# Performance work log

Measured on AMD Instinct MI355X. Metric: run time of the kernel, lower is better.

## Reference

```python
import jax, jax.numpy as jnp
import numpy as np

H = 512          # hidden_size
SH = 120         # scoring_net_hidden_size
B = 1024         # batch
S = 64           # num_sentences


def setup_inputs() -> dict:
    key = jax.random.key(0)
    ks = jax.random.split(key, 12)
    sc = 0.05
    return {
        "C": jax.random.normal(ks[0], (B, S, H), jnp.float32),
        "Q": jax.random.normal(ks[1], (B, 1, H), jnp.float32),
        "prev_M": jax.random.normal(ks[2], (B, 1, H), jnp.float32),
        # scoring network params: fc1: 4H -> SH, fc2: SH -> 1
        "fc1_w": jax.random.normal(ks[3], (SH, 4 * H), jnp.float32) * sc,
        "fc1_b": jnp.zeros((SH,), jnp.float32),
        "fc2_w": jax.random.normal(ks[4], (1, SH), jnp.float32) * sc,
        "fc2_b": jnp.zeros((1,), jnp.float32),
        # GRU params (torch layout: rows ordered r, z, n)
        "W_ih": jax.random.normal(ks[5], (3 * H, H), jnp.float32) * sc,
        "W_hh": jax.random.normal(ks[6], (3 * H, H), jnp.float32) * sc,
        "b_ih": jnp.zeros((3 * H,), jnp.float32),
        "b_hh": jnp.zeros((3 * H,), jnp.float32),
    }


def reference(C, Q, prev_M, fc1_w, fc1_b, fc2_w, fc2_b, W_ih, W_hh, b_ih, b_hh):
    # --- scoring network (arch=1 feature vector) ---
    feat = jnp.concatenate(
        [C * Q, C * prev_M, jnp.abs(C - Q), jnp.abs(C - prev_M)], axis=2
    )  # [B, S, 4H]
    h1 = jnp.tanh(jnp.einsum("bsf,kf->bsk", feat, fc1_w) + fc1_b)
    G = jax.nn.sigmoid((jnp.einsum("bsk,ok->bso", h1, fc2_w) + fc2_b)[..., 0])  # [B, S]

    # --- gated GRU memory update over sentences ---
    xg_all = jnp.einsum("bsh,gh->bsg", C, W_ih) + b_ih  # [B, S, 3H] precomputed input gates

    def step(h, inp):
        xg, g = inp  # xg: [B, 3H], g: [B]
        hg = h @ W_hh.T + b_hh
        xr, xz, xn = jnp.split(xg, 3, axis=-1)
        hr, hz, hn = jnp.split(hg, 3, axis=-1)
        r = jax.nn.sigmoid(xr + hr)
        z = jax.nn.sigmoid(xz + hz)
        n = jnp.tanh(xn + r * hn)
        h_gru = (1.0 - z) * n + z * h          # standard torch GRU update
        g = g[:, None]
        h_new = g * h_gru + (1.0 - g) * h      # episodic gating
        return h_new, None

    h0 = jnp.zeros((C.shape[0], H), C.dtype)
    h_final, _ = jax.lax.scan(step, h0, (xg_all.transpose(1, 0, 2), G.T))
    return h_final[:, None, :]  # [B, 1, H]
```

## Files before the change

kernel.cpp:

```cpp
#include <hip/hip_runtime.h>
#include <hip/hip_bf16.h>

#define H_ 512
#define SH_ 120
#define B_ 1024
#define S_ 64

typedef __bf16 bf16x8 __attribute__((ext_vector_type(8)));
typedef float floatx4 __attribute__((ext_vector_type(4)));

__device__ __forceinline__ float bf2f(ushort u) {
    union { unsigned int i; float f; } v; v.i = ((unsigned int)u) << 16; return v.f;
}
__device__ __forceinline__ ushort f2bf(float f) {
    union { float f; unsigned int i; } v; v.f = f;
    unsigned int x = v.i;
    unsigned int r = (x + 0x7fffu + ((x >> 16) & 1u)) >> 16;
    return (ushort)r;
}

__device__ __attribute__((aligned(64))) unsigned g_prog[256];

__global__ __launch_bounds__(256) void prep_w(
    const float* __restrict__ fc1w, ushort* __restrict__ fc1wb,
    const float* __restrict__ Wih,  ushort* __restrict__ Wihb,
    const float* __restrict__ Whh,  ushort* __restrict__ Whhb)
{
    const int stride = gridDim.x * blockDim.x;
    const int tid = blockIdx.x * blockDim.x + threadIdx.x;
    for (int i = tid; i < 61440; i += stride) {
        const float4 v = ((const float4*)fc1w)[i];
        ushort4 o; o.x = f2bf(v.x); o.y = f2bf(v.y); o.z = f2bf(v.z); o.w = f2bf(v.w);
        ((ushort4*)fc1wb)[i] = o;
    }
    for (int i = tid; i < 196608; i += stride) {
        const float4 v = ((const float4*)Wih)[i];
        ushort4 o; o.x = f2bf(v.x); o.y = f2bf(v.y); o.z = f2bf(v.z); o.w = f2bf(v.w);
        ((ushort4*)Wihb)[i] = o;
    }
    for (int i = tid; i < 196608; i += stride) {
        const float4 v = ((const float4*)Whh)[i];
        ushort4 o; o.x = f2bf(v.x); o.y = f2bf(v.y); o.z = f2bf(v.z); o.w = f2bf(v.w);
        ((ushort4*)Whhb)[i] = o;
    }
}

__global__ __launch_bounds__(256) void g_kernel(
    const float* __restrict__ C, const float* __restrict__ Q,
    const float* __restrict__ M, const ushort* __restrict__ fc1wb,
    const float* __restrict__ fc1b, const float* __restrict__ fc2w,
    const float* __restrict__ fc2b, float* __restrict__ G)
{
    __shared__ float qrow[H_];
    __shared__ float mrow[H_];
    __shared__ __align__(16) ushort featT[64 * 72];
    __shared__ __align__(16) ushort wT[128 * 72];
    __shared__ float h1s[64 * 132];

    const int b = blockIdx.x;
    const int t = threadIdx.x;
    for (int i = t; i < H_; i += 256) { qrow[i] = Q[(size_t)b * H_ + i]; mrow[i] = M[(size_t)b * H_ + i]; }

    const int wrow = t >> 1;
    const int wc0  = (t & 1) * 32;
    if (wrow >= SH_) {
        uint4* dst = (uint4*)&wT[wrow * 72 + wc0];
        const uint4 z = {0u, 0u, 0u, 0u};
        dst[0] = z; dst[1] = z; dst[2] = z; dst[3] = z;
    }
    __syncthreads();

    const int lane = t & 63;
    const int wv   = t >> 6;
    const int quad = lane >> 4;
    const int l15  = lane & 15;
    const int arow = wv * 16 + l15;
    const int s    = t >> 2;
    const int c0   = (t & 3) * 16;

    floatx4 acc[8];
#pragma unroll
    for (int i = 0; i < 8; ++i) acc[i] = (floatx4){0.f, 0.f, 0.f, 0.f};

    for (int hc = 0; hc < H_; hc += 64) {
        float cr[16];
        {
            const float4* csrc = (const float4*)(C + ((size_t)b * S_ + s) * H_ + hc + c0);
            *(float4*)&cr[0]  = csrc[0];
            *(float4*)&cr[4]  = csrc[1];
            *(float4*)&cr[8]  = csrc[2];
            *(float4*)&cr[12] = csrc[3];
        }
#pragma unroll
        for (int seg = 0; seg < 4; ++seg) {
#pragma unroll
            for (int u = 0; u < 16; ++u) {
                const int kk = c0 + u;
                const float c = cr[u];
                const float o = (seg == 0 || seg == 2) ? qrow[hc + kk] : mrow[hc + kk];
                const float v = (seg < 2) ? c * o : fabsf(c - o);
                featT[s * 72 + kk] = f2bf(v);
            }
            if (wrow < SH_) {
                const uint4* src = (const uint4*)(fc1wb + (size_t)wrow * (4 * H_) + seg * H_ + hc + wc0);
                uint4* dst = (uint4*)&wT[wrow * 72 + wc0];
                dst[0] = src[0]; dst[1] = src[1]; dst[2] = src[2]; dst[3] = src[3];
            }
            __syncthreads();
#pragma unroll
            for (int ks = 0; ks < 64; ks += 32) {
                const int ao = ks + quad * 8;
                const bf16x8 af = *(const bf16x8*)&featT[arow * 72 + ao];
#pragma unroll
                for (int nt = 0; nt < 8; ++nt) {
                    const bf16x8 bfr = *(const bf16x8*)&wT[(nt * 16 + l15) * 72 + ao];
                    acc[nt] = __builtin_amdgcn_mfma_f32_16x16x32_bf16(af, bfr, acc[nt], 0, 0, 0);
                }
            }
            __syncthreads();
        }
    }

#pragma unroll
    for (int nt = 0; nt < 8; ++nt) {
        const int col = nt * 16 + l15;
        const float bias = (col < SH_) ? fc1b[col] : 0.f;
#pragma unroll
        for (int r = 0; r < 4; ++r) {
            const int row = wv * 16 + quad * 4 + r;
            h1s[row * 132 + col] = (col < SH_) ? tanhf(acc[nt][r] + bias) : 0.f;
        }
    }
    __syncthreads();
    {
        const int part = t & 3;
        float sum = 0.f;
        for (int k = part; k < SH_; k += 4) sum += h1s[s * 132 + k] * fc2w[k];
        sum += __shfl_xor(sum, 1);
        sum += __shfl_xor(sum, 2);
        if (part == 0) {
            const float logit = sum + fc2b[0];
            G[(size_t)b * S_ + s] = 1.f / (1.f + expf(-logit));
        }
    }
}

__global__ __launch_bounds__(256) void scan_all(
    const float* __restrict__ C, const ushort* __restrict__ Wihb,
    const ushort* __restrict__ Whhb, const float* __restrict__ bih,
    const float* __restrict__ bhh, const float* __restrict__ G,
    uint* __restrict__ hp0, uint* __restrict__ hp1,
    float* __restrict__ out)
{
    __shared__ __align__(16) ushort Whh_s[96 * 520];
    __shared__ __align__(16) ushort As[3 * 64 * 72];
    __shared__ __align__(16) ushort Wih_s[96 * 72];

    const int bx = blockIdx.x;
    const int jt = bx >> 4;
    const int bt = ((bx & 7) << 1) | ((bx >> 3) & 1);
    const int jb = jt * 32;
    const int bb = bt * 64;
    const int t  = threadIdx.x;
    const int lane = t & 63;
    const int wv   = t >> 6;
    const int quad = lane >> 4;
    const int l15  = lane & 15;
    const int arow = wv * 16 + l15;
    const int crow = t >> 2;
    const int cc0  = (t & 3) * 16;
    const int hrow = t >> 2;
    const int hseg = t & 3;

    const unsigned vbase = __hip_atomic_load(&g_prog[(bt << 4) + jt],
                                             __ATOMIC_RELAXED, __HIP_MEMORY_SCOPE_AGENT);

#pragma unroll
    for (int i = 0; i < 24; ++i) {
        const int gid = i * 256 + t;
        const int row = gid >> 6;
        const int grp = gid & 63;
        const int grow = (row >> 5) * H_ + jb + (row & 31);
        *(uint4*)&Whh_s[row * 520 + grp * 8] =
            *(const uint4*)(Whhb + (size_t)grow * H_ + grp * 8);
    }

    float br_[2], bz_[2], bxn_[2], bhn_[2];
#pragma unroll
    for (int nt = 0; nt < 2; ++nt) {
        const int j = jb + nt * 16 + l15;
        br_[nt]  = bih[j] + bhh[j];
        bz_[nt]  = bih[H_ + j] + bhh[H_ + j];
        bxn_[nt] = bih[2 * H_ + j];
        bhn_[nt] = bhh[2 * H_ + j];
    }

    const int hold_kc  = (jb >> 6) << 6;
    const int hold_off = jb & 63;

    const uint* hr = hp0;
    uint*       hw = hp1;

    float cr[16];
    unsigned long long hreg[8];
    uint4 wreg[3];

    auto load_cw = [&](int tstep, int kc) {
        const float4* src = (const float4*)(C + ((size_t)(bb + crow) * S_ + tstep) * H_ + kc + cc0);
        *(float4*)&cr[0]  = src[0];
        *(float4*)&cr[4]  = src[1];
        *(float4*)&cr[8]  = src[2];
        *(float4*)&cr[12] = src[3];
#pragma unroll
        for (int i = 0; i < 3; ++i) {
            const int gid = i * 256 + t;
            const int row = gid >> 3;
            const int grp = gid & 7;
            const int grow = (row >> 5) * H_ + jb + (row & 31);
            wreg[i] = *(const uint4*)(Wihb + (size_t)grow * H_ + kc + grp * 8);
        }
    };
    auto load_h = [&](int kc) {
        const unsigned long long* src = (const unsigned long long*)
            (hr + (size_t)(bb + hrow) * H_ + kc + hseg * 16);
#pragma unroll
        for (int i = 0; i < 8; ++i)
            hreg[i] = __hip_atomic_load(src + i, __ATOMIC_RELAXED, __HIP_MEMORY_SCOPE_AGENT);
    };
    auto write_lds = [&]() {
        __align__(16) ushort cb[16];
#pragma unroll
        for (int u = 0; u < 16; ++u) cb[u] = f2bf(cr[u]);
        uint4* d = (uint4*)&As[crow * 72 + cc0];
        d[0] = ((uint4*)cb)[0]; d[1] = ((uint4*)cb)[1];
        uint hiu[8], lou[8];
#pragma unroll
        for (int i = 0; i < 8; ++i) {
            const uint p0 = (uint)(hreg[i] & 0xFFFFFFFFull);
            const uint p1 = (uint)(hreg[i] >> 32);
            hiu[i] = (p0 >> 16) | (p1 & 0xFFFF0000u);
            lou[i] = (p0 & 0xFFFFu) | (p1 << 16);
        }
        uint4* dh = (uint4*)&As[1 * 4608 + hrow * 72 + hseg * 16];
        dh[0] = *(uint4*)&hiu[0]; dh[1] = *(uint4*)&hiu[4];
        uint4* dl = (uint4*)&As[2 * 4608 + hrow * 72 + hseg * 16];
        dl[0] = *(uint4*)&lou[0]; dl[1] = *(uint4*)&lou[4];
#pragma unroll
        for (int i = 0; i < 3; ++i) {
            const int gid = i * 256 + t;
            const int row = gid >> 3;
            const int grp = gid & 7;
            *(uint4*)&Wih_s[row * 72 + grp * 8] = wreg[i];
        }
    };

    load_cw(0, 0);
    load_h(0);

    for (int tstep = 0; tstep < S_; ++tstep) {
        float g_[4];
#pragma unroll
        for (int r4 = 0; r4 < 4; ++r4)
            g_[r4] = G[(size_t)(bb + wv * 16 + quad * 4 + r4) * S_ + tstep];

        floatx4 acc_r[2], acc_z[2], acc_xn[2], acc_hn[2];
#pragma unroll
        for (int i = 0; i < 2; ++i) {
            acc_r[i] = (floatx4){0.f,0.f,0.f,0.f}; acc_z[i]  = (floatx4){0.f,0.f,0.f,0.f};
            acc_xn[i]= (floatx4){0.f,0.f,0.f,0.f}; acc_hn[i] = (floatx4){0.f,0.f,0.f,0.f};
        }
        float hold_[2][4];

        for (int kc = 0; kc < H_; kc += 64) {
            write_lds();
            __syncthreads();
            const int kn = kc + 64;
            if (kn < H_) { load_cw(tstep, kn); load_h(kn); }
            if (kc == hold_kc) {
#pragma unroll
                for (int nt = 0; nt < 2; ++nt)
#pragma unroll
                    for (int r4 = 0; r4 < 4; ++r4) {
                        const int trow = wv * 16 + quad * 4 + r4;
                        const int col  = hold_off + nt * 16 + l15;
                        hold_[nt][r4] = bf2f(As[1 * 4608 + trow * 72 + col]) +
                                        bf2f(As[2 * 4608 + trow * 72 + col]);
                    }
            }
#pragma unroll
            for (int ks = 0; ks < 64; ks += 32) {
                const int ao = ks + quad * 8;
                const bf16x8 a_c  = *(const bf16x8*)&As[0 * 4608 + arow * 72 + ao];
                const bf16x8 a_hh = *(const bf16x8*)&As[1 * 4608 + arow * 72 + ao];
                const bf16x8 a_hl = *(const bf16x8*)&As[2 * 4608 + arow * 72 + ao];
#pragma unroll
                for (int nt = 0; nt < 2; ++nt) {
                    const int jj = nt * 16 + l15;
                    const bf16x8 ih_r = *(const bf16x8*)&Wih_s[(0 * 32 + jj) * 72 + ao];
                    const bf16x8 ih_z = *(const bf16x8*)&Wih_s[(1 * 32 + jj) * 72 + ao];
                    const bf16x8 ih_n = *(const bf16x8*)&Wih_s[(2 * 32 + jj) * 72 + ao];
                    const bf16x8 hh_r = *(const bf16x8*)&Whh_s[(0 * 32 + jj) * 520 + kc + ao];
                    const bf16x8 hh_z = *(const bf16x8*)&Whh_s[(1 * 32 + jj) * 520 + kc + ao];
                    const bf16x8 hh_n = *(const bf16x8*)&Whh_s[(2 * 32 + jj) * 520 + kc + ao];
                    acc_r[nt]  = __builtin_amdgcn_mfma_f32_16x16x32_bf16(a_c,  ih_r, acc_r[nt],  0, 0, 0);
                    acc_r[nt]  = __builtin_amdgcn_mfma_f32_16x16x32_bf16(a_hh, hh_r, acc_r[nt],  0, 0, 0);
                    acc_r[nt]  = __builtin_amdgcn_mfma_f32_16x16x32_bf16(a_hl, hh_r, acc_r[nt],  0, 0, 0);
                    acc_z[nt]  = __builtin_amdgcn_mfma_f32_16x16x32_bf16(a_c,  ih_z, acc_z[nt],  0, 0, 0);
                    acc_z[nt]  = __builtin_amdgcn_mfma_f32_16x16x32_bf16(a_hh, hh_z, acc_z[nt],  0, 0, 0);
                    acc_z[nt]  = __builtin_amdgcn_mfma_f32_16x16x32_bf16(a_hl, hh_z, acc_z[nt],  0, 0, 0);
                    acc_xn[nt] = __builtin_amdgcn_mfma_f32_16x16x32_bf16(a_c,  ih_n, acc_xn[nt], 0, 0, 0);
                    acc_hn[nt] = __builtin_amdgcn_mfma_f32_16x16x32_bf16(a_hh, hh_n, acc_hn[nt], 0, 0, 0);
                    acc_hn[nt] = __builtin_amdgcn_mfma_f32_16x16x32_bf16(a_hl, hh_n, acc_hn[nt], 0, 0, 0);
                }
            }
            __syncthreads();
        }

        const int last = (tstep == S_ - 1);
#pragma unroll
        for (int nt = 0; nt < 2; ++nt) {
            const int j = jb + nt * 16 + l15;
#pragma unroll
            for (int r4 = 0; r4 < 4; ++r4) {
                const int b = bb + wv * 16 + quad * 4 + r4;
                const size_t idx = (size_t)b * H_ + j;
                const float hold = hold_[nt][r4];
                const float g = g_[r4];
                const float rg = 1.f / (1.f + expf(-(acc_r[nt][r4] + br_[nt])));
                const float zg = 1.f / (1.f + expf(-(acc_z[nt][r4] + bz_[nt])));
                const float ng = tanhf(acc_xn[nt][r4] + bxn_[nt] + rg * (acc_hn[nt][r4] + bhn_[nt]));
                const float hgru = (1.f - zg) * ng + zg * hold;
                const float hnew = g * hgru + (1.f - g) * hold;
                const ushort hb = f2bf(hnew);
                const ushort hl = f2bf(hnew - bf2f(hb));
                __hip_atomic_store(&hw[idx], ((uint)hb << 16) | (uint)hl,
                                   __ATOMIC_RELAXED, __HIP_MEMORY_SCOPE_AGENT);
                if (last) out[idx] = hnew;
            }
        }
        if (last) break;

        {
            uint* tmp = hw; hw = (uint*)hr; hr = (const uint*)tmp;
        }
        load_cw(tstep + 1, 0);

        asm volatile("s_waitcnt vmcnt(0)" ::: "memory");
        __syncthreads();
        if (t == 0)
            __hip_atomic_store(&g_prog[(bt << 4) + jt], vbase + (unsigned)(tstep + 1),
                               __ATOMIC_RELAXED, __HIP_MEMORY_SCOPE_AGENT);
        if (wv == 0) {
            const unsigned tgt = vbase + (unsigned)(tstep + 1);
            const int slot = (bt << 4) + (t & 15);
            while (true) {
                const unsigned v = __hip_atomic_load(&g_prog[slot],
                                                     __ATOMIC_RELAXED, __HIP_MEMORY_SCOPE_AGENT);
                if (__all(v >= tgt)) break;
                __builtin_amdgcn_s_sleep(4);
            }
        }
        __syncthreads();
        load_h(0);
    }
}

extern "C" void kernel_launch(void* const* d_in, const int* in_sizes, int n_in,
                              void* d_out, int out_size, void* d_ws, size_t ws_size,
                              hipStream_t stream) {
    (void)in_sizes; (void)n_in; (void)out_size; (void)ws_size;
    const float* C    = (const float*)d_in[0];
    const float* Q    = (const float*)d_in[1];
    const float* M    = (const float*)d_in[2];
    const float* fc1w = (const float*)d_in[3];
    const float* fc1b = (const float*)d_in[4];
    const float* fc2w = (const float*)d_in[5];
    const float* fc2b = (const float*)d_in[6];
    const float* Wih  = (const float*)d_in[7];
    const float* Whh  = (const float*)d_in[8];
    const float* bih  = (const float*)d_in[9];
    const float* bhh  = (const float*)d_in[10];
    float* out = (float*)d_out;

    char* ws = (char*)d_ws;
    float* Gbuf  = (float*)ws;
    uint*  hp0   = (uint*)(ws + 262144);
    uint*  hp1   = (uint*)(ws + 262144 + 2097152);
    ushort* fc1wb = (ushort*)(ws + 4456448);
    ushort* Wihb  = (ushort*)(ws + 4947968);
    ushort* Whhb  = (ushort*)(ws + 6520832);

    hipMemsetAsync(hp0, 0, 2097152, stream);

    prep_w<<<256, 256, 0, stream>>>(fc1w, fc1wb, Wih, Wihb, Whh, Whhb);
    g_kernel<<<B_, 256, 0, stream>>>(C, Q, M, fc1wb, fc1b, fc2w, fc2b, Gbuf);
    scan_all<<<256, 256, 0, stream>>>(C, Wihb, Whhb, bih, bhh, Gbuf,
                                      hp0, hp1, out);
}
```

Baseline: 1.482 ms.

## Double-buffer A tiles, load W_ih fragments to registers, retile waves over 32x48 outputs

Restructures the scan's inner loop. The A operands (C, h-high, h-low) now go into two LDS buffers, so the next k-chunk is written while the current one is consumed, leaving one barrier per chunk instead of two. W_ih fragments are read straight into MFMA B registers rather than staged through LDS. Waves are retiled so each covers 32 rows by 48 gate columns, reusing A fragments across two row tiles. Accumulators pass through LDS to the epilogue layout, which adds a barrier and extra LDS traffic, and the spin-wait sleep is shortened.

```diff
diff --git a/kernel.cpp b/kernel.cpp
--- a/kernel.cpp
+++ b/kernel.cpp
@@ -153,8 +153,9 @@
     float* __restrict__ out)
 {
     __shared__ __align__(16) ushort Whh_s[96 * 520];
-    __shared__ __align__(16) ushort As[3 * 64 * 72];
-    __shared__ __align__(16) ushort Wih_s[96 * 72];
+    __shared__ __align__(16) char  smem_u[55296];
+    ushort* AsU = (ushort*)smem_u;
+    float*  gs  = (float*)smem_u;
 
     const int bx = blockIdx.x;
     const int jt = bx >> 4;
@@ -166,7 +167,8 @@
     const int wv   = t >> 6;
     const int quad = lane >> 4;
     const int l15  = lane & 15;
-    const int arow = wv * 16 + l15;
+    const int mh   = wv >> 1;
+    const int cset = wv & 1;
     const int crow = t >> 2;
     const int cc0  = (t & 3) * 16;
     const int hrow = t >> 2;
@@ -203,22 +205,14 @@
 
     float cr[16];
     unsigned long long hreg[8];
-    uint4 wreg[3];
-
-    auto load_cw = [&](int tstep, int kc) {
+    bf16x8 bi[3][2];
+
+    auto load_c = [&](int tstep, int kc) {
         const float4* src = (const float4*)(C + ((size_t)(bb + crow) * S_ + tstep) * H_ + kc + cc0);
         *(float4*)&cr[0]  = src[0];
         *(float4*)&cr[4]  = src[1];
         *(float4*)&cr[8]  = src[2];
         *(float4*)&cr[12] = src[3];
-#pragma unroll
-        for (int i = 0; i < 3; ++i) {
-            const int gid = i * 256 + t;
-            const int row = gid >> 3;
-            const int grp = gid & 7;
-            const int grow = (row >> 5) * H_ + jb + (row & 31);
-            wreg[i] = *(const uint4*)(Wihb + (size_t)grow * H_ + kc + grp * 8);
-        }
     };
     auto load_h = [&](int kc) {
         const unsigned long long* src = (const unsigned long long*)
@@ -227,11 +221,22 @@
         for (int i = 0; i < 8; ++i)
             hreg[i] = __hip_atomic_load(src + i, __ATOMIC_RELAXED, __HIP_MEMORY_SCOPE_AGENT);
     };
-    auto write_lds = [&]() {
+    auto loadBi = [&](int kc) {
+#pragma unroll
+        for (int ct = 0; ct < 3; ++ct) {
+            const int ctg = cset * 3 + ct;
+            const size_t wrow = (size_t)((ctg >> 1) * H_ + jb + (ctg & 1) * 16 + l15) * H_;
+#pragma unroll
+            for (int ks2 = 0; ks2 < 2; ++ks2)
+                bi[ct][ks2] = *(const bf16x8*)(Wihb + wrow + kc + ks2 * 32 + quad * 8);
+        }
+    };
+    auto write_As = [&](int buf) {
+        ushort* base = AsU + buf * 13824;
         __align__(16) ushort cb[16];
 #pragma unroll
         for (int u = 0; u < 16; ++u) cb[u] = f2bf(cr[u]);
-        uint4* d = (uint4*)&As[crow * 72 + cc0];
+        uint4* d = (uint4*)&base[crow * 72 + cc0];
         d[0] = ((uint4*)cb)[0]; d[1] = ((uint4*)cb)[1];
         uint hiu[8], lou[8];
 #pragma unroll
@@ -241,21 +246,15 @@
             hiu[i] = (p0 >> 16) | (p1 & 0xFFFF0000u);
             lou[i] = (p0 & 0xFFFFu) | (p1 << 16);
         }
-        uint4* dh = (uint4*)&As[1 * 4608 + hrow * 72 + hseg * 16];
+        uint4* dh = (uint4*)&base[4608 + hrow * 72 + hseg * 16];
         dh[0] = *(uint4*)&hiu[0]; dh[1] = *(uint4*)&hiu[4];
-        uint4* dl = (uint4*)&As[2 * 4608 + hrow * 72 + hseg * 16];
+        uint4* dl = (uint4*)&base[9216 + hrow * 72 + hseg * 16];
         dl[0] = *(uint4*)&lou[0]; dl[1] = *(uint4*)&lou[4];
-#pragma unroll
-        for (int i = 0; i < 3; ++i) {
-            const int gid = i * 256 + t;
-            const int row = gid >> 3;
-            const int grp = gid & 7;
-            *(uint4*)&Wih_s[row * 72 + grp * 8] = wreg[i];
-        }
     };
 
-    load_cw(0, 0);
-    load_h(0);
+    load_c(0, 0); loadBi(0); load_h(0);
+    write_As(0);
+    __syncthreads();
 
     for (int tstep = 0; tstep < S_; ++tstep) {
         float g_[4];
@@ -263,58 +262,84 @@
         for (int r4 = 0; r4 < 4; ++r4)
             g_[r4] = G[(size_t)(bb + wv * 16 + quad * 4 + r4) * S_ + tstep];
 
-        floatx4 acc_r[2], acc_z[2], acc_xn[2], acc_hn[2];
-#pragma unroll
-        for (int i = 0; i < 2; ++i) {
-            acc_r[i] = (floatx4){0.f,0.f,0.f,0.f}; acc_z[i]  = (floatx4){0.f,0.f,0.f,0.f};
-            acc_xn[i]= (floatx4){0.f,0.f,0.f,0.f}; acc_hn[i] = (floatx4){0.f,0.f,0.f,0.f};
+        floatx4 accA[2][3], accB[2][2];
+#pragma unroll
+        for (int rf = 0; rf < 2; ++rf) {
+#pragma unroll
+            for (int i = 0; i < 3; ++i) accA[rf][i] = (floatx4){0.f, 0.f, 0.f, 0.f};
+#pragma unroll
+            for (int i = 0; i < 2; ++i) accB[rf][i] = (floatx4){0.f, 0.f, 0.f, 0.f};
         }
         float hold_[2][4];
 
         for (int kc = 0; kc < H_; kc += 64) {
-            write_lds();
+            const int cur = (kc >> 6) & 1;
+            const int kn  = kc + 64;
+            if (kn < H_) { load_c(tstep, kn); load_h(kn); }
+            const ushort* Ac = AsU + cur * 13824;
+            const ushort* Ah = Ac + 4608;
+            const ushort* Al = Ac + 9216;
+#pragma unroll
+            for (int ks2 = 0; ks2 < 2; ++ks2) {
+                const int ao = ks2 * 32 + quad * 8;
+                bf16x8 a_c[2], a_hh[2], a_hl[2];
+#pragma unroll
+                for (int rf = 0; rf < 2; ++rf) {
+                    const int ai = (mh * 32 + rf * 16 + l15) * 72 + ao;
+                    a_c[rf]  = *(const bf16x8*)&Ac[ai];
+                    a_hh[rf] = *(const bf16x8*)&Ah[ai];
+                    a_hl[rf] = *(const bf16x8*)&Al[ai];
+                }
+#pragma unroll
+                for (int ct = 0; ct < 3; ++ct) {
+                    const int ctg = cset * 3 + ct;
+                    const bf16x8 bh = *(const bf16x8*)
+                        &Whh_s[((ctg >> 1) * 32 + (ctg & 1) * 16 + l15) * 520 + kc + ao];
+#pragma unroll
+                    for (int rf = 0; rf < 2; ++rf) {
+                        if (ct >= 1 && cset == 1) {
+                            accA[rf][ct]     = __builtin_amdgcn_mfma_f32_16x16x32_bf16(a_c[rf],  bi[ct][ks2], accA[rf][ct],     0, 0, 0);
+                            accB[rf][ct - 1] = __builtin_amdgcn_mfma_f32_16x16x32_bf16(a_hh[rf], bh,          accB[rf][ct - 1], 0, 0, 0);
+                            accB[rf][ct - 1] = __builtin_amdgcn_mfma_f32_16x16x32_bf16(a_hl[rf], bh,          accB[rf][ct - 1], 0, 0, 0);
+                        } else {
+                            accA[rf][ct] = __builtin_amdgcn_mfma_f32_16x16x32_bf16(a_c[rf],  bi[ct][ks2], accA[rf][ct], 0, 0, 0);
+                            accA[rf][ct] = __builtin_amdgcn_mfma_f32_16x16x32_bf16(a_hh[rf], bh,          accA[rf][ct], 0, 0, 0);
+                            accA[rf][ct] = __builtin_amdgcn_mfma_f32_16x16x32_bf16(a_hl[rf], bh,          accA[rf][ct], 0, 0, 0);
+                        }
+                    }
+                }
+            }
+            if (kn < H_) { loadBi(kn); write_As(cur ^ 1); }
+            if (kc == hold_kc) {
+#pragma unroll
+                for (int nt = 0; nt < 2; ++nt)
+#pragma unroll
+                    for (int r4 = 0; r4 < 4; ++r4) {
+                        const int ai = (wv * 16 + quad * 4 + r4) * 72 + hold_off + nt * 16 + l15;
+                        hold_[nt][r4] = bf2f(Ah[ai]) + bf2f(Al[ai]);
+                    }
+            }
             __syncthreads();
-            const int kn = kc + 64;
-            if (kn < H_) { load_cw(tstep, kn); load_h(kn); }
-            if (kc == hold_kc) {
-#pragma unroll
-                for (int nt = 0; nt < 2; ++nt)
-#pragma unroll
-                    for (int r4 = 0; r4 < 4; ++r4) {
-                        const int trow = wv * 16 + quad * 4 + r4;
-                        const int col  = hold_off + nt * 16 + l15;
-                        hold_[nt][r4] = bf2f(As[1 * 4608 + trow * 72 + col]) +
-                                        bf2f(As[2 * 4608 + trow * 72 + col]);
-                    }
-            }
-#pragma unroll
-            for (int ks = 0; ks < 64; ks += 32) {
-                const int ao = ks + quad * 8;
-                const bf16x8 a_c  = *(const bf16x8*)&As[0 * 4608 + arow * 72 + ao];
-                const bf16x8 a_hh = *(const bf16x8*)&As[1 * 4608 + arow * 72 + ao];
-                const bf16x8 a_hl = *(const bf16x8*)&As[2 * 4608 + arow * 72 + ao];
-#pragma unroll
-                for (int nt = 0; nt < 2; ++nt) {
-                    const int jj = nt * 16 + l15;
-                    const bf16x8 ih_r = *(const bf16x8*)&Wih_s[(0 * 32 + jj) * 72 + ao];
-                    const bf16x8 ih_z = *(const bf16x8*)&Wih_s[(1 * 32 + jj) * 72 + ao];
-                    const bf16x8 ih_n = *(const bf16x8*)&Wih_s[(2 * 32 + jj) * 72 + ao];
-                    const bf16x8 hh_r = *(const bf16x8*)&Whh_s[(0 * 32 + jj) * 520 + kc + ao];
-                    const bf16x8 hh_z = *(const bf16x8*)&Whh_s[(1 * 32 + jj) * 520 + kc + ao];
-                    const bf16x8 hh_n = *(const bf16x8*)&Whh_s[(2 * 32 + jj) * 520 + kc + ao];
-                    acc_r[nt]  = __builtin_amdgcn_mfma_f32_16x16x32_bf16(a_c,  ih_r, acc_r[nt],  0, 0, 0);
-                    acc_r[nt]  = __builtin_amdgcn_mfma_f32_16x16x32_bf16(a_hh, hh_r, acc_r[nt],  0, 0, 0);
-                    acc_r[nt]  = __builtin_amdgcn_mfma_f32_16x16x32_bf16(a_hl, hh_r, acc_r[nt],  0, 0, 0);
-                    acc_z[nt]  = __builtin_amdgcn_mfma_f32_16x16x32_bf16(a_c,  ih_z, acc_z[nt],  0, 0, 0);
-                    acc_z[nt]  = __builtin_amdgcn_mfma_f32_16x16x32_bf16(a_hh, hh_z, acc_z[nt],  0, 0, 0);
-                    acc_z[nt]  = __builtin_amdgcn_mfma_f32_16x16x32_bf16(a_hl, hh_z, acc_z[nt],  0, 0, 0);
-                    acc_xn[nt] = __builtin_amdgcn_mfma_f32_16x16x32_bf16(a_c,  ih_n, acc_xn[nt], 0, 0, 0);
-                    acc_hn[nt] = __builtin_amdgcn_mfma_f32_16x16x32_bf16(a_hh, hh_n, acc_hn[nt], 0, 0, 0);
-                    acc_hn[nt] = __builtin_amdgcn_mfma_f32_16x16x32_bf16(a_hl, hh_n, acc_hn[nt], 0, 0, 0);
-                }
-            }
-            __syncthreads();
-        }
+        }
+
+#pragma unroll
+        for (int rf = 0; rf < 2; ++rf)
+#pragma unroll
+        for (int ct = 0; ct < 3; ++ct) {
+            const int ctg = cset * 3 + ct;
+            const int go  = ctg >> 1;
+            const int col = (ctg & 1) * 16 + l15;
+            const int rbase = mh * 32 + rf * 16 + quad * 4;
+#pragma unroll
+            for (int r = 0; r < 4; ++r)
+                gs[go * 2304 + (rbase + r) * 36 + col] = accA[rf][ct][r];
+            if (ct >= 1 && cset == 1) {
+#pragma unroll
+                for (int r = 0; r < 4; ++r)
+                    gs[3 * 2304 + (rbase + r) * 36 + col] = accB[rf][ct - 1][r];
+            }
+        }
+        __syncthreads();
 
         const int last = (tstep == S_ - 1);
 #pragma unroll
@@ -322,13 +347,19 @@
             const int j = jb + nt * 16 + l15;
 #pragma unroll
             for (int r4 = 0; r4 < 4; ++r4) {
-                const int b = bb + wv * 16 + quad * 4 + r4;
+                const int row = wv * 16 + quad * 4 + r4;
+                const int b = bb + row;
                 const size_t idx = (size_t)b * H_ + j;
+                const int gidx = row * 36 + nt * 16 + l15;
+                const float rrv = gs[0 * 2304 + gidx];
+                const float zzv = gs[1 * 2304 + gidx];
+                const float xnv = gs[2 * 2304 + gidx];
+                const float hnv = gs[3 * 2304 + gidx];
                 const float hold = hold_[nt][r4];
                 const float g = g_[r4];
-                const float rg = 1.f / (1.f + expf(-(acc_r[nt][r4] + br_[nt])));
-                const float zg = 1.f / (1.f + expf(-(acc_z[nt][r4] + bz_[nt])));
-                const float ng = tanhf(acc_xn[nt][r4] + bxn_[nt] + rg * (acc_hn[nt][r4] + bhn_[nt]));
+                const float rg = 1.f / (1.f + expf(-(rrv + br_[nt])));
+                const float zg = 1.f / (1.f + expf(-(zzv + bz_[nt])));
+                const float ng = tanhf(xnv + bxn_[nt] + rg * (hnv + bhn_[nt]));
                 const float hgru = (1.f - zg) * ng + zg * hold;
                 const float hnew = g * hgru + (1.f - g) * hold;
                 const ushort hb = f2bf(hnew);
@@ -340,10 +371,10 @@
         }
         if (last) break;
 
-        {
-            uint* tmp = hw; hw = (uint*)hr; hr = (const uint*)tmp;
-        }
-        load_cw(tstep + 1, 0);
+        { uint* tmp = hw; hw = (uint*)hr; hr = (const uint*)tmp; }
+
+        load_c(tstep + 1, 0);
+        loadBi(0);
 
         asm volatile("s_waitcnt vmcnt(0)" ::: "memory");
         __syncthreads();
@@ -357,11 +388,14 @@
                 const unsigned v = __hip_atomic_load(&g_prog[slot],
                                                      __ATOMIC_RELAXED, __HIP_MEMORY_SCOPE_AGENT);
                 if (__all(v >= tgt)) break;
-                __builtin_amdgcn_s_sleep(4);
+                __builtin_amdgcn_s_sleep(2);
             }
         }
         __syncthreads();
+
         load_h(0);
+        write_As(0);
+        __syncthreads();
     }
 }
 
```

New measurement: 1.541 ms. +4.0%, slower.
